# Kernel tuning notes

Measured on AMD Instinct MI355X. Metric: run time of the kernel, lower is better.

The kernel has to match this reference:

```python
import jax, jax.numpy as jnp
import numpy as np

DIM = 1024
NUM_HEADS = 16
DIM_HEAD = 64
INNER = NUM_HEADS * DIM_HEAD  # 1024
SCALE = DIM_HEAD ** -0.5


def setup_inputs() -> dict:
    key = jax.random.key(0)
    ks = jax.random.split(key, 8)
    B, SQ, SK = 2, 2048, 4096
    x = jax.random.normal(ks[0], (B, SQ, DIM), dtype=jnp.float32)
    context = jax.random.normal(ks[1], (B, SK, DIM), dtype=jnp.float32)
    # LayerNorm params
    ln_gamma = jnp.ones((DIM,), jnp.float32)
    ln_beta = jnp.zeros((DIM,), jnp.float32)
    # Linear weights, stored as [in, out] so y = x @ W (torch Linear weight transposed)
    w_q = jax.random.normal(ks[2], (DIM, INNER), dtype=jnp.float32) / np.sqrt(DIM)
    w_kv = jax.random.normal(ks[3], (DIM, 2 * INNER), dtype=jnp.float32) / np.sqrt(DIM)
    w_out = jax.random.normal(ks[4], (INNER, DIM), dtype=jnp.float32) / np.sqrt(INNER)
    b_out = jnp.zeros((DIM,), jnp.float32)
    # torch init is 0.0 (tanh(0)=0); use a nonzero value so output/grads are nontrivial
    gate = jnp.array([0.5], jnp.float32)
    return {"x": x, "context": context, "ln_gamma": ln_gamma, "ln_beta": ln_beta,
            "w_q": w_q, "w_kv": w_kv, "w_out": w_out, "b_out": b_out, "gate": gate}


def _layernorm(x, gamma, beta, eps=1e-5):
    mu = jnp.mean(x, axis=-1, keepdims=True)
    var = jnp.mean(jnp.square(x - mu), axis=-1, keepdims=True)
    return (x - mu) * jax.lax.rsqrt(var + eps) * gamma + beta


def reference(x, context, ln_gamma, ln_beta, w_q, w_kv, w_out, b_out, gate):
    B, SQ, _ = x.shape
    SK = context.shape[1]
    xn = _layernorm(x, ln_gamma, ln_beta)
    q = (xn @ w_q).reshape(B, SQ, NUM_HEADS, DIM_HEAD)
    kv = context @ w_kv
    k, v = jnp.split(kv, 2, axis=-1)
    k = k.reshape(B, SK, NUM_HEADS, DIM_HEAD)
    v = v.reshape(B, SK, NUM_HEADS, DIM_HEAD)
    # scores: [B, H, SQ, SK]
    scores = jnp.einsum('bqhd,bkhd->bhqk', q * SCALE, k)
    attn = jax.nn.softmax(scores, axis=-1)
    out = jnp.einsum('bhqk,bkhd->bqhd', attn, v).reshape(B, SQ, INNER)
    out = out @ w_out + b_out
    return out * jnp.tanh(gate[0])
```

## Files before the change

kernel.cpp:

```cpp
#include <hip/hip_runtime.h>
#include <hip/hip_bf16.h>
#include <stdint.h>

#define DIMM  1024
#define NHEAD 16
#define DHEAD 64
#define BB    2
#define SQL   2048
#define SKL   4096
#define KVW   2048
#define NT    (SKL / 64)

typedef __attribute__((ext_vector_type(8))) short short8;
typedef __attribute__((ext_vector_type(4))) float f32x4;
typedef __attribute__((ext_vector_type(16))) float f32x16;
typedef __attribute__((ext_vector_type(4))) unsigned short us4;

typedef const __attribute__((address_space(1))) uint32_t gu32_t;
typedef __attribute__((address_space(3))) uint32_t lu32_t;

#define GLDS16(gp, lp) __builtin_amdgcn_global_load_lds((gu32_t*)(gp), (lu32_t*)(lp), 16, 0, 0)

static __device__ __forceinline__ unsigned short f2bf(float f) {
  union { float f; uint32_t u; } v; v.f = f;
  uint32_t r = v.u + 0x7fffu + ((v.u >> 16) & 1u);
  return (unsigned short)(r >> 16);
}

__global__ __launch_bounds__(256) void k_transpose_cast(const float* __restrict__ in,
                                                        unsigned short* __restrict__ out,
                                                        int K, int N) {
  __shared__ float tile[32][33];
  int n0 = blockIdx.x * 32, k0 = blockIdx.y * 32;
  int tx = threadIdx.x, ty = threadIdx.y;
  #pragma unroll
  for (int i = 0; i < 4; i++)
    tile[ty + i * 8][tx] = in[(size_t)(k0 + ty + i * 8) * N + n0 + tx];
  __syncthreads();
  #pragma unroll
  for (int i = 0; i < 4; i++)
    out[(size_t)(n0 + ty + i * 8) * K + k0 + tx] = f2bf(tile[tx][ty + i * 8]);
}

__global__ __launch_bounds__(256) void k_ln(const float* __restrict__ x,
                                            const float* __restrict__ gamma,
                                            const float* __restrict__ beta,
                                            unsigned short* __restrict__ out) {
  const int row = blockIdx.x, tid = threadIdx.x;
  const float* xr = x + (size_t)row * DIMM;
  float4 v = *(const float4*)(xr + tid * 4);
  float s = v.x + v.y + v.z + v.w;
  float ss = v.x * v.x + v.y * v.y + v.z * v.z + v.w * v.w;
  #pragma unroll
  for (int m = 1; m < 64; m <<= 1) {
    s += __shfl_xor(s, m);
    ss += __shfl_xor(ss, m);
  }
  __shared__ float red[8];
  const int wid = tid >> 6, lane = tid & 63;
  if (lane == 0) { red[wid] = s; red[4 + wid] = ss; }
  __syncthreads();
  s = red[0] + red[1] + red[2] + red[3];
  ss = red[4] + red[5] + red[6] + red[7];
  float mu = s * (1.0f / DIMM);
  float var = ss * (1.0f / DIMM) - mu * mu;
  float rstd = rsqrtf(var + 1e-5f);
  float4 g = *(const float4*)(gamma + tid * 4);
  float4 bt = *(const float4*)(beta + tid * 4);
  us4 o;
  o.x = f2bf((v.x - mu) * rstd * g.x + bt.x);
  o.y = f2bf((v.y - mu) * rstd * g.y + bt.y);
  o.z = f2bf((v.z - mu) * rstd * g.z + bt.z);
  o.w = f2bf((v.w - mu) * rstd * g.w + bt.w);
  *(us4*)(out + (size_t)row * DIMM + tid * 4) = o;
}

__global__ __launch_bounds__(256) void k_proj(const float* __restrict__ ctx,
                                              const unsigned short* __restrict__ XN,
                                              const unsigned short* __restrict__ WKVT,
                                              const unsigned short* __restrict__ WQT,
                                              unsigned short* __restrict__ KVB,
                                              unsigned short* __restrict__ QB) {
  __shared__ unsigned short lA[2][128 * 32];
  __shared__ unsigned short lB[2][128 * 32];
  const int tid = threadIdx.x;
  const int wid = tid >> 6, lane = tid & 63;
  const int kg = lane >> 4, lr = lane & 15;
  const int wr = wid >> 1, wc = wid & 1;
  const int K = 1024, nt = 32;

  const int bid = blockIdx.x;
  const int xcd = bid & 7;
  const int idx = bid >> 3;
  const bool isQ = (idx >= 128);
  int im, in_, N;
  const unsigned short* Bw;
  unsigned short* Cout;
  if (isQ) { int q = idx - 128; im = xcd * 4 + (q & 3); in_ = q >> 2; Bw = WQT;  Cout = QB;  N = 1024; }
  else     {                    im = xcd * 8 + (idx & 7); in_ = idx >> 3; Bw = WKVT; Cout = KVB; N = 2048; }
  const size_t baseB = (size_t)in_ * 128 * K;
  const unsigned short* Abf = XN + (size_t)im * 128 * K;
  const float* Af = ctx + (size_t)im * 128 * K;

  int ed[2], grow[2], gcol[2];
  #pragma unroll
  for (int j = 0; j < 2; j++) {
    int e = wid * 1024 + j * 512 + lane * 8;
    ed[j] = e;
    int row = e >> 5;
    grow[j] = row;
    gcol[j] = (((e >> 3) & 3) ^ ((row >> 1) & 3)) << 3;
  }
  uint32_t awoff[4];
  #pragma unroll
  for (int p = 0; p < 4; p++) {
    int row = p * 32 + (tid >> 3);
    int g = (tid & 7) >> 1;
    awoff[p] = (uint32_t)(row * 64 + ((g ^ ((row >> 1) & 3)) << 4) + (tid & 1) * 8);
  }

  f32x4 acc[4][4];
  #pragma unroll
  for (int m = 0; m < 4; m++)
    #pragma unroll
    for (int n = 0; n < 4; n++) {
      f32x4 z = {0.0f, 0.0f, 0.0f, 0.0f};
      acc[m][n] = z;
    }

  float4 va[4];
  auto STAGE_B = [&](int bufi, int t) {
    int k0 = t << 5;
    #pragma unroll
    for (int j = 0; j < 2; j++)
      GLDS16(Bw + baseB + (size_t)grow[j] * K + k0 + gcol[j], &lB[bufi][ed[j]]);
  };
  auto STAGE_A_Q = [&](int bufi, int t) {
    int k0 = t << 5;
    #pragma unroll
    for (int j = 0; j < 2; j++)
      GLDS16(Abf + (size_t)grow[j] * K + k0 + gcol[j], &lA[bufi][ed[j]]);
  };
  auto LOAD_A_F32 = [&](int t) {
    int k0 = t << 5;
    #pragma unroll
    for (int p = 0; p < 4; p++)
      va[p] = *(const float4*)(Af + (size_t)(p * 32 + (tid >> 3)) * K + k0 + (tid & 7) * 4);
  };
  auto WRITE_A_F32 = [&](int bufi) {
    #pragma unroll
    for (int p = 0; p < 4; p++) {
      uint32_t lo, hi;
      asm("v_cvt_pk_bf16_f32 %0, %1, %2" : "=v"(lo) : "v"(va[p].x), "v"(va[p].y));
      asm("v_cvt_pk_bf16_f32 %0, %1, %2" : "=v"(hi) : "v"(va[p].z), "v"(va[p].w));
      uint2 w2; w2.x = lo; w2.y = hi;
      *(uint2*)((char*)&lA[bufi][0] + awoff[p]) = w2;
    }
  };
  auto COMPUTE = [&](int bufi) {
    short8 a[4], b[4];
    #pragma unroll
    for (int m = 0; m < 4; m++) {
      int row = wr * 64 + m * 16 + lr;
      a[m] = *(const short8*)&lA[bufi][row * 32 + ((kg ^ ((row >> 1) & 3)) << 3)];
    }
    #pragma unroll
    for (int n = 0; n < 4; n++) {
      int row = wc * 64 + n * 16 + lr;
      b[n] = *(const short8*)&lB[bufi][row * 32 + ((kg ^ ((row >> 1) & 3)) << 3)];
    }
    #pragma unroll
    for (int m = 0; m < 4; m++)
      #pragma unroll
      for (int n = 0; n < 4; n++)
        acc[m][n] = __builtin_amdgcn_mfma_f32_16x16x32_bf16(a[m], b[n], acc[m][n], 0, 0, 0);
  };

  int buf = 0;
  if (isQ) {
    STAGE_A_Q(0, 0); STAGE_B(0, 0);
    __syncthreads();
    for (int t = 0; t < nt; t++) {
      if (t + 1 < nt) { STAGE_A_Q(buf ^ 1, t + 1); STAGE_B(buf ^ 1, t + 1); }
      COMPUTE(buf);
      __syncthreads();
      buf ^= 1;
    }
  } else {
    LOAD_A_F32(0); STAGE_B(0, 0); WRITE_A_F32(0);
    __syncthreads();
    for (int t = 0; t < nt; t++) {
      if (t + 1 < nt) { LOAD_A_F32(t + 1); STAGE_B(buf ^ 1, t + 1); }
      COMPUTE(buf);
      if (t + 1 < nt) WRITE_A_F32(buf ^ 1);
      __syncthreads();
      buf ^= 1;
    }
  }

  const int r0 = im * 128 + wr * 64;
  const int c0 = in_ * 128 + wc * 64;
  #pragma unroll
  for (int m = 0; m < 4; m++)
    #pragma unroll
    for (int n = 0; n < 4; n++)
      #pragma unroll
      for (int j = 0; j < 4; j++)
        Cout[(size_t)(r0 + m * 16 + kg * 4 + j) * N + c0 + n * 16 + lr] = f2bf(acc[m][n][j]);
}

__global__ __launch_bounds__(256) void k_out(const unsigned short* __restrict__ A,
                                             const unsigned short* __restrict__ BT,
                                             float* __restrict__ C,
                                             const float* __restrict__ bias,
                                             const float* __restrict__ gate) {
  __shared__ unsigned short lA[2][64 * 32];
  __shared__ unsigned short lB[2][128 * 32];
  const int tid = threadIdx.x;
  const int wid = tid >> 6, lane = tid & 63;
  const int kg = lane >> 4, lr = lane & 15;
  const int wr = wid >> 1, wc = wid & 1;
  const int K = 1024, nt = 32, N = 1024;

  const int bid = blockIdx.x;
  const int xcd = bid & 7;
  const int idx = bid >> 3;
  const int im = xcd * 8 + (idx & 7);
  const int in_ = idx >> 3;
  const size_t baseA = (size_t)im * 64 * K;
  const size_t baseB = (size_t)in_ * 128 * K;

  int eA, arow, acol;
  {
    int e = tid * 8;
    eA = e;
    int row = e >> 5;
    arow = row; acol = (((e >> 3) & 3) ^ ((row >> 1) & 3)) << 3;
  }
  int eB[2], brow[2], bcol[2];
  #pragma unroll
  for (int j = 0; j < 2; j++) {
    int e = tid * 8 + j * 2048;
    eB[j] = e;
    int row = e >> 5;
    brow[j] = row; bcol[j] = (((e >> 3) & 3) ^ ((row >> 1) & 3)) << 3;
  }

  f32x4 acc[2][4];
  #pragma unroll
  for (int m = 0; m < 2; m++)
    #pragma unroll
    for (int n = 0; n < 4; n++) {
      f32x4 z = {0.0f, 0.0f, 0.0f, 0.0f};
      acc[m][n] = z;
    }

  auto STAGE = [&](int bufi, int t) {
    int k0 = t << 5;
    GLDS16(A + baseA + (size_t)arow * K + k0 + acol, &lA[bufi][eA]);
    #pragma unroll
    for (int j = 0; j < 2; j++)
      GLDS16(BT + baseB + (size_t)brow[j] * K + k0 + bcol[j], &lB[bufi][eB[j]]);
  };

  STAGE(0, 0);
  __syncthreads();
  int buf = 0;
  for (int t = 0; t < nt; t++) {
    if (t + 1 < nt) STAGE(buf ^ 1, t + 1);
    short8 a[2], b[4];
    #pragma unroll
    for (int m = 0; m < 2; m++) {
      int row = wr * 32 + m * 16 + lr;
      a[m] = *(const short8*)&lA[buf][row * 32 + ((kg ^ ((row >> 1) & 3)) << 3)];
    }
    #pragma unroll
    for (int n = 0; n < 4; n++) {
      int row = wc * 64 + n * 16 + lr;
      b[n] = *(const short8*)&lB[buf][row * 32 + ((kg ^ ((row >> 1) & 3)) << 3)];
    }
    #pragma unroll
    for (int m = 0; m < 2; m++)
      #pragma unroll
      for (int n = 0; n < 4; n++)
        acc[m][n] = __builtin_amdgcn_mfma_f32_16x16x32_bf16(a[m], b[n], acc[m][n], 0, 0, 0);
    __syncthreads();
    buf ^= 1;
  }

  const int r0 = im * 64 + wr * 32;
  const int c0 = in_ * 128 + wc * 64;
  float gl = tanhf(gate[0]);
  #pragma unroll
  for (int m = 0; m < 2; m++)
    #pragma unroll
    for (int n = 0; n < 4; n++)
      #pragma unroll
      for (int j = 0; j < 4; j++) {
        int col = c0 + n * 16 + lr;
        C[(size_t)(r0 + m * 16 + kg * 4 + j) * N + col] = (acc[m][n][j] + bias[col]) * gl;
      }
}

__global__ __launch_bounds__(256, 4) void k_attn(const unsigned short* __restrict__ Q,
                                                 const unsigned short* __restrict__ KV,
                                                 unsigned short* __restrict__ O) {
  __shared__ unsigned short sK[2][64 * 64];
  __shared__ unsigned short sV[2][64 * 64];

  const int tid = threadIdx.x;
  const int wave = tid >> 6, lane = tid & 63;
  const int wq = wave & 1, wk = wave >> 1;
  const int l31 = lane & 31, hi = lane >> 5;

  const int wid_b = blockIdx.x;
  const int work = (wid_b & 7) * 128 + (wid_b >> 3);
  const int qb = work & 31, bh = work >> 5;
  const int b = bh >> 4, h = bh & 15;

  const unsigned short* Qp = Q + (size_t)b * SQL * DIMM + h * DHEAD;
  const unsigned short* Kp = KV + (size_t)b * SKL * KVW + h * DHEAD;
  const unsigned short* Vp = Kp + DIMM;

  const int qr0 = qb * 64 + wq * 32;

  const unsigned short* ksrc[2]; int kdst[2];
  const unsigned short* vsrc[2]; int vdst[2];
  #pragma unroll
  for (int j = 0; j < 2; j++) {
    int e = (tid + j * 256) * 8;
    int row = e >> 6;
    int col = (((e >> 3) & 7) ^ (row & 7)) << 3;
    ksrc[j] = Kp + (size_t)row * KVW + col;
    kdst[j] = e;
    int g = tid + j * 256;
    int key = (g >> 5) * 4 + ((g >> 1) & 3);
    int d0v = ((g >> 3) & 3) * 16 + (g & 1) * 8;
    vsrc[j] = Vp + (size_t)key * KVW + d0v;
    vdst[j] = g * 8;
  }

  auto STAGE = [&](int bufi, int kt) {
    size_t off = (size_t)kt * 64 * KVW;
    #pragma unroll
    for (int j = 0; j < 2; j++) GLDS16(ksrc[j] + off, &sK[bufi][kdst[j]]);
    #pragma unroll
    for (int j = 0; j < 2; j++) GLDS16(vsrc[j] + off, &sV[bufi][vdst[j]]);
  };

  short8 qa[4];
  #pragma unroll
  for (int t = 0; t < 4; t++) {
    short8 v = *(const short8*)(Qp + (size_t)(qr0 + l31) * DIMM + t * 16 + hi * 8);
    #pragma unroll
    for (int j = 0; j < 8; j++) {
      union { float f; uint32_t u; } c;
      c.u = ((uint32_t)(unsigned short)v[j]) << 16;
      v[j] = (short)f2bf(c.f * 0.1803368801111f);
    }
    qa[t] = v;
  }

  f32x16 oacc[2];
  #pragma unroll
  for (int d2 = 0; d2 < 2; d2++)
    #pragma unroll
    for (int r = 0; r < 16; r++) oacc[d2][r] = 0.0f;
  float rs = 0.0f;

  const uint32_t sVb0 = (uint32_t)(size_t)(lu32_t*)&sV[0][0] +
                        (uint32_t)(hi * 1024 + ((lane >> 4) & 1) * 128 + (lane & 15) * 8);

  STAGE(0, 0);
  __syncthreads();

  union u4s8 { uint32_t u[4]; short8 s; };

  int buf = 0;
  for (int kt = 0; kt < NT; kt++) {
    if (kt + 1 < NT) STAGE(buf ^ 1, kt + 1);

    short8 kbf[4];
    {
      int row = wk * 32 + l31;
      #pragma unroll
      for (int t = 0; t < 4; t++) {
        int gl = t * 2 + hi;
        kbf[t] = *(const short8*)&sK[buf][row * 64 + ((gl ^ (row & 7)) << 3)];
      }
    }

    f32x16 sc;
    #pragma unroll
    for (int r = 0; r < 16; r++) sc[r] = 0.0f;
    __builtin_amdgcn_s_setprio(1);
    #pragma unroll
    for (int t = 0; t < 4; t++)
      sc = __builtin_amdgcn_mfma_f32_32x32x16_bf16(kbf[t], qa[t], sc, 0, 0, 0);
    __builtin_amdgcn_s_setprio(0);

    float p[16];
    #pragma unroll
    for (int r = 0; r < 16; r++) {
      p[r] = __builtin_amdgcn_exp2f(sc[r]);
      rs += p[r];
    }
    uint32_t w[8];
    #pragma unroll
    for (int i = 0; i < 8; i++)
      asm("v_cvt_pk_bf16_f32 %0, %1, %2" : "=v"(w[i]) : "v"(p[2 * i]), "v"(p[2 * i + 1]));
    asm("v_permlane32_swap_b32 %0, %1" : "+v"(w[0]), "+v"(w[2]));
    asm("v_permlane32_swap_b32 %0, %1" : "+v"(w[1]), "+v"(w[3]));
    asm("v_permlane32_swap_b32 %0, %1" : "+v"(w[4]), "+v"(w[6]));
    asm("v_permlane32_swap_b32 %0, %1" : "+v"(w[5]), "+v"(w[7]));
    u4s8 paf[2];
    paf[0].u[0] = w[0]; paf[0].u[1] = w[1]; paf[0].u[2] = w[2]; paf[0].u[3] = w[3];
    paf[1].u[0] = w[4]; paf[1].u[1] = w[5]; paf[1].u[2] = w[6]; paf[1].u[3] = w[7];

    u4s8 vb[2][2];
    {
      uint32_t tb = sVb0 + (uint32_t)(buf * 8192 + wk * 4096);
      #pragma unroll
      for (int d2 = 0; d2 < 2; d2++)
        #pragma unroll
        for (int ks = 0; ks < 2; ks++) {
          uint2 t0, t1;
          uint32_t a0 = tb + (uint32_t)(ks * 2048 + d2 * 256);
          asm volatile("ds_read_b64_tr_b16 %0, %1" : "=v"(t0) : "v"(a0));
          asm volatile("ds_read_b64_tr_b16 %0, %1" : "=v"(t1) : "v"(a0 + 512u));
          vb[d2][ks].u[0] = t0.x; vb[d2][ks].u[1] = t0.y;
          vb[d2][ks].u[2] = t1.x; vb[d2][ks].u[3] = t1.y;
        }
    }
    asm volatile("s_waitcnt lgkmcnt(0)" ::: "memory");
    __builtin_amdgcn_sched_barrier(0);

    __builtin_amdgcn_s_setprio(1);
    #pragma unroll
    for (int d2 = 0; d2 < 2; d2++)
      #pragma unroll
      for (int ks = 0; ks < 2; ks++)
        oacc[d2] = __builtin_amdgcn_mfma_f32_32x32x16_bf16(paf[ks].s, vb[d2][ks].s, oacc[d2], 0, 0, 0);
    __builtin_amdgcn_s_setprio(0);

    __syncthreads();
    buf ^= 1;
  }

  float* sRed = (float*)&sK[0][0];
  float* sRs  = (float*)&sV[0][0];
  if (wk == 1) {
    #pragma unroll
    for (int d2 = 0; d2 < 2; d2++)
      #pragma unroll
      for (int r = 0; r < 16; r++)
        sRed[((wq * 2 + d2) * 16 + r) * 64 + lane] = oacc[d2][r];
    sRs[wq * 64 + lane] = rs;
  }
  __syncthreads();
  if (wk == 0) {
    #pragma unroll
    for (int d2 = 0; d2 < 2; d2++)
      #pragma unroll
      for (int r = 0; r < 16; r++)
        oacc[d2][r] += sRed[((wq * 2 + d2) * 16 + r) * 64 + lane];
    float rs2 = rs + sRs[wq * 64 + lane];
    float t = rs2 + __shfl_xor(rs2, 32);
    float inv = 1.0f / t;
    float rq[16];
    #pragma unroll
    for (int r = 0; r < 16; r++) {
      int rho = (r & 3) + 8 * (r >> 2) + 4 * hi;
      rq[r] = __shfl(inv, rho);
    }
    unsigned short* Op = O + (size_t)b * SQL * DIMM + h * DHEAD;
    #pragma unroll
    for (int d2 = 0; d2 < 2; d2++)
      #pragma unroll
      for (int r = 0; r < 16; r++) {
        int rho = (r & 3) + 8 * (r >> 2) + 4 * hi;
        Op[(size_t)(qr0 + rho) * DIMM + d2 * 32 + l31] = f2bf(oacc[d2][r] * rq[r]);
      }
  }
}

extern "C" void kernel_launch(void* const* d_in, const int* in_sizes, int n_in,
                              void* d_out, int out_size, void* d_ws, size_t ws_size,
                              hipStream_t stream) {
  (void)in_sizes; (void)n_in; (void)out_size; (void)ws_size;
  const float* x     = (const float*)d_in[0];
  const float* ctx   = (const float*)d_in[1];
  const float* gamma = (const float*)d_in[2];
  const float* beta  = (const float*)d_in[3];
  const float* w_q   = (const float*)d_in[4];
  const float* w_kv  = (const float*)d_in[5];
  const float* w_out = (const float*)d_in[6];
  const float* b_out = (const float*)d_in[7];
  const float* gate  = (const float*)d_in[8];
  float* out = (float*)d_out;
  char* ws = (char*)d_ws;

  unsigned short* XN   = (unsigned short*)(ws);
  unsigned short* QB   = (unsigned short*)(ws + (8ull  << 20));
  unsigned short* KVB  = (unsigned short*)(ws + (32ull << 20));
  unsigned short* OB   = (unsigned short*)(ws + (64ull << 20));
  unsigned short* WQT  = (unsigned short*)(ws + (72ull << 20));
  unsigned short* WKVT = (unsigned short*)(ws + (74ull << 20));
  unsigned short* WOT  = (unsigned short*)(ws + (78ull << 20));

  k_transpose_cast<<<dim3(32, 32), dim3(32, 8), 0, stream>>>(w_q, WQT, 1024, 1024);
  k_transpose_cast<<<dim3(64, 32), dim3(32, 8), 0, stream>>>(w_kv, WKVT, 1024, 2048);
  k_transpose_cast<<<dim3(32, 32), dim3(32, 8), 0, stream>>>(w_out, WOT, 1024, 1024);
  k_ln<<<dim3(4096), dim3(256), 0, stream>>>(x, gamma, beta, XN);
  k_proj<<<dim3(1280), dim3(256), 0, stream>>>(ctx, XN, WKVT, WQT, KVB, QB);
  k_attn<<<dim3(1024), dim3(256), 0, stream>>>(QB, KVB, OB);
  k_out<<<dim3(512), dim3(256), 0, stream>>>(OB, WOT, out, b_out, gate);
}
```

Baseline: 211.7 us.

## Load K directly to registers in attention and merge weight transpose launches

The attention kernel now reads K fragments from global memory straight into registers, prefetching one tile ahead with two register sets. This replaces the LDS staging for K. The loop is unrolled by two with compile-time buffer indices, the s_setprio hints are dropped, and LDS use shrinks since only V stays in shared memory. The three weight transpose-cast launches are merged into one kernel that picks its matrix from the block index, which saves launch overhead. K is now read from global per wave rather than once per block, so the two key-halves each load their own rows and there is more register pressure.

```diff
diff --git a/kernel.cpp b/kernel.cpp
--- a/kernel.cpp
+++ b/kernel.cpp
@@ -27,12 +27,21 @@
   return (unsigned short)(r >> 16);
 }
 
-__global__ __launch_bounds__(256) void k_transpose_cast(const float* __restrict__ in,
-                                                        unsigned short* __restrict__ out,
-                                                        int K, int N) {
+__global__ __launch_bounds__(256) void k_wprep(const float* __restrict__ wq,
+                                               const float* __restrict__ wkv,
+                                               const float* __restrict__ wot,
+                                               unsigned short* __restrict__ WQT,
+                                               unsigned short* __restrict__ WKVT,
+                                               unsigned short* __restrict__ WOT) {
   __shared__ float tile[32][33];
-  int n0 = blockIdx.x * 32, k0 = blockIdx.y * 32;
-  int tx = threadIdx.x, ty = threadIdx.y;
+  const int bid = blockIdx.x;
+  const float* in; unsigned short* out; int N, bx, by;
+  if (bid < 1024)      {               in = wq;  out = WQT;  N = 1024; bx = bid & 31; by = bid >> 5; }
+  else if (bid < 3072) { int l = bid - 1024; in = wkv; out = WKVT; N = 2048; bx = l & 63; by = l >> 6; }
+  else                 { int l = bid - 3072; in = wot; out = WOT;  N = 1024; bx = l & 31; by = l >> 5; }
+  const int K = 1024;
+  const int n0 = bx * 32, k0 = by * 32;
+  const int tx = threadIdx.x, ty = threadIdx.y;
   #pragma unroll
   for (int i = 0; i < 4; i++)
     tile[ty + i * 8][tx] = in[(size_t)(k0 + ty + i * 8) * N + n0 + tx];
@@ -305,8 +314,8 @@
 __global__ __launch_bounds__(256, 4) void k_attn(const unsigned short* __restrict__ Q,
                                                  const unsigned short* __restrict__ KV,
                                                  unsigned short* __restrict__ O) {
-  __shared__ unsigned short sK[2][64 * 64];
   __shared__ unsigned short sV[2][64 * 64];
+  __shared__ float sRs[128];
 
   const int tid = threadIdx.x;
   const int wave = tid >> 6, lane = tid & 63;
@@ -324,28 +333,28 @@
 
   const int qr0 = qb * 64 + wq * 32;
 
-  const unsigned short* ksrc[2]; int kdst[2];
   const unsigned short* vsrc[2]; int vdst[2];
   #pragma unroll
   for (int j = 0; j < 2; j++) {
-    int e = (tid + j * 256) * 8;
-    int row = e >> 6;
-    int col = (((e >> 3) & 7) ^ (row & 7)) << 3;
-    ksrc[j] = Kp + (size_t)row * KVW + col;
-    kdst[j] = e;
     int g = tid + j * 256;
     int key = (g >> 5) * 4 + ((g >> 1) & 3);
     int d0v = ((g >> 3) & 3) * 16 + (g & 1) * 8;
     vsrc[j] = Vp + (size_t)key * KVW + d0v;
     vdst[j] = g * 8;
   }
-
-  auto STAGE = [&](int bufi, int kt) {
+  auto STAGE_V = [&](int bufi, int kt) {
     size_t off = (size_t)kt * 64 * KVW;
     #pragma unroll
-    for (int j = 0; j < 2; j++) GLDS16(ksrc[j] + off, &sK[bufi][kdst[j]]);
-    #pragma unroll
     for (int j = 0; j < 2; j++) GLDS16(vsrc[j] + off, &sV[bufi][vdst[j]]);
+  };
+
+  const unsigned short* Kw = Kp + (size_t)(wk * 32 + l31) * KVW + hi * 8;
+  short8 ka[4], kb_[4];
+  auto LOADK = [&](short8* dst, int kt) {
+    size_t off = (size_t)kt * 64 * KVW;
+    #pragma unroll
+    for (int t = 0; t < 4; t++)
+      dst[t] = *(const short8*)(Kw + off + t * 16);
   };
 
   short8 qa[4];
@@ -371,33 +380,15 @@
   const uint32_t sVb0 = (uint32_t)(size_t)(lu32_t*)&sV[0][0] +
                         (uint32_t)(hi * 1024 + ((lane >> 4) & 1) * 128 + (lane & 15) * 8);
 
-  STAGE(0, 0);
-  __syncthreads();
-
   union u4s8 { uint32_t u[4]; short8 s; };
 
-  int buf = 0;
-  for (int kt = 0; kt < NT; kt++) {
-    if (kt + 1 < NT) STAGE(buf ^ 1, kt + 1);
-
-    short8 kbf[4];
-    {
-      int row = wk * 32 + l31;
-      #pragma unroll
-      for (int t = 0; t < 4; t++) {
-        int gl = t * 2 + hi;
-        kbf[t] = *(const short8*)&sK[buf][row * 64 + ((gl ^ (row & 7)) << 3)];
-      }
-    }
-
+  auto BODY = [&](const short8* kf, int BUF) {
     f32x16 sc;
     #pragma unroll
     for (int r = 0; r < 16; r++) sc[r] = 0.0f;
-    __builtin_amdgcn_s_setprio(1);
     #pragma unroll
     for (int t = 0; t < 4; t++)
-      sc = __builtin_amdgcn_mfma_f32_32x32x16_bf16(kbf[t], qa[t], sc, 0, 0, 0);
-    __builtin_amdgcn_s_setprio(0);
+      sc = __builtin_amdgcn_mfma_f32_32x32x16_bf16(kf[t], qa[t], sc, 0, 0, 0);
 
     float p[16];
     #pragma unroll
@@ -419,7 +410,7 @@
 
     u4s8 vb[2][2];
     {
-      uint32_t tb = sVb0 + (uint32_t)(buf * 8192 + wk * 4096);
+      uint32_t tb = sVb0 + (uint32_t)(BUF * 8192 + wk * 4096);
       #pragma unroll
       for (int d2 = 0; d2 < 2; d2++)
         #pragma unroll
@@ -435,20 +426,27 @@
     asm volatile("s_waitcnt lgkmcnt(0)" ::: "memory");
     __builtin_amdgcn_sched_barrier(0);
 
-    __builtin_amdgcn_s_setprio(1);
     #pragma unroll
     for (int d2 = 0; d2 < 2; d2++)
       #pragma unroll
       for (int ks = 0; ks < 2; ks++)
         oacc[d2] = __builtin_amdgcn_mfma_f32_32x32x16_bf16(paf[ks].s, vb[d2][ks].s, oacc[d2], 0, 0, 0);
-    __builtin_amdgcn_s_setprio(0);
-
+  };
+
+  LOADK(ka, 0);
+  STAGE_V(0, 0);
+  __syncthreads();
+
+  for (int kt = 0; kt < NT; kt += 2) {
+    if (kt + 1 < NT) { LOADK(kb_, kt + 1); STAGE_V(1, kt + 1); }
+    BODY(ka, 0);
     __syncthreads();
-    buf ^= 1;
-  }
-
-  float* sRed = (float*)&sK[0][0];
-  float* sRs  = (float*)&sV[0][0];
+    if (kt + 2 < NT) { LOADK(ka, kt + 2); STAGE_V(0, kt + 2); }
+    BODY(kb_, 1);
+    __syncthreads();
+  }
+
+  float* sRed = (float*)&sV[0][0];
   if (wk == 1) {
     #pragma unroll
     for (int d2 = 0; d2 < 2; d2++)
@@ -508,9 +506,7 @@
   unsigned short* WKVT = (unsigned short*)(ws + (74ull << 20));
   unsigned short* WOT  = (unsigned short*)(ws + (78ull << 20));
 
-  k_transpose_cast<<<dim3(32, 32), dim3(32, 8), 0, stream>>>(w_q, WQT, 1024, 1024);
-  k_transpose_cast<<<dim3(64, 32), dim3(32, 8), 0, stream>>>(w_kv, WKVT, 1024, 2048);
-  k_transpose_cast<<<dim3(32, 32), dim3(32, 8), 0, stream>>>(w_out, WOT, 1024, 1024);
+  k_wprep<<<dim3(4096), dim3(32, 8), 0, stream>>>(w_q, w_kv, w_out, WQT, WKVT, WOT);
   k_ln<<<dim3(4096), dim3(256), 0, stream>>>(x, gamma, beta, XN);
   k_proj<<<dim3(1280), dim3(256), 0, stream>>>(ctx, XN, WKVT, WQT, KVB, QB);
   k_attn<<<dim3(1024), dim3(256), 0, stream>>>(QB, KVB, OB);
```

New measurement: 306.9 us. +45.0%, slower.
